# Kernel optimization log

Measured on AMD Instinct MI355X. Metric: run time of the kernel, lower is better.

The kernel has to match this reference:

```python
import jax, jax.numpy as jnp
import numpy as np

SEQ = 512; WIN = [4, 4, 4]; INNER = 5; DM = 256; H = 4; DK = 64; NEG = -1e9

def _all_sizes():
    s = [SEQ]
    for w in WIN:
        s.append(s[-1] // w)
    return s

def _build_mask():
    # Pyraformer get_mask: intra-scale band (inner_size) + inter-scale parent/child links.
    sizes = _all_sizes(); N = sum(sizes)
    starts = np.cumsum([0] + sizes)
    allow = np.zeros((N, N), bool)
    iw = INNER // 2
    for li, sz in enumerate(sizes):
        st = int(starts[li])
        for i in range(st, st + sz):
            allow[i, max(i - iw, st):min(i + iw + 1, st + sz)] = True
    for li in range(1, len(sizes)):
        st = int(starts[li])
        for i in range(st, st + sizes[li]):
            ls = int(starts[li - 1]) + (i - st) * WIN[li - 1]
            rs = st if i == st + sizes[li] - 1 else int(starts[li - 1]) + (i - st + 1) * WIN[li - 1]
            allow[i, ls:rs] = True
            allow[ls:rs, i] = True
    return jnp.asarray(~allow)  # True = blocked

def _build_indexes():
    # Pyraformer refer_points: for each base position, index of its node at every scale.
    sizes = _all_sizes(); starts = np.cumsum([0] + sizes)
    idx = np.zeros((SEQ, len(sizes)), np.int32)
    for i in range(SEQ):
        cur = i
        idx[i, 0] = cur
        for j in range(1, len(sizes)):
            inner = cur - int(starts[j - 1])
            cur = int(starts[j]) + min(inner // WIN[j - 1], sizes[j] - 1)
            idx[i, j] = cur
    return jnp.asarray(idx)

def _pos_enc(L, D):
    pos = np.arange(L)[:, None]
    div = np.exp(np.arange(0, D, 2) * (-np.log(10000.0) / D))
    pe = np.zeros((L, D), np.float32)
    pe[:, 0::2] = np.sin(pos * div)
    pe[:, 1::2] = np.cos(pos * div)
    return jnp.asarray(pe)

MASK = _build_mask()
INDEXES = _build_indexes()
PE = _pos_enc(SEQ, DM)
DN = ('NCH', 'OIH', 'NCH')

def _ln(x, g, b, eps=1e-5):
    m = x.mean(-1, keepdims=True)
    v = ((x - m) ** 2).mean(-1, keepdims=True)
    return (x - m) * jax.lax.rsqrt(v + eps) * g + b

def _forward(x_enc, x_mark, W_val, W_time, b_time, W_down, b_down, W_conv, b_conv, bn_g, bn_b, W_up, b_up, ln_c_g, ln_c_b, Wq, bq, Wk, bk, Wv, bv, Wo, bo, ln1_g, ln1_b, W1f, b1f, W2f, b2f, ln2_g, ln2_b, Wp, bp):
    B = x_enc.shape[0]
    # DataEmbedding: circular k=3 token conv + time-feature linear + fixed positional
    xt = jnp.pad(x_enc.transpose(0, 2, 1), ((0, 0), (0, 0), (1, 1)), mode='wrap')
    val = jax.lax.conv_general_dilated(xt, W_val, (1,), 'VALID', dimension_numbers=DN).transpose(0, 2, 1)
    emb = val + x_mark @ W_time + b_time + PE[None]  # [B, SEQ, DM]
    # CSCM Bottleneck_Construct: down-proj, strided conv pooling per scale, up-proj, concat, LN
    t = (emb @ W_down + b_down).transpose(0, 2, 1)  # [B, 64, SEQ]
    pooled = []
    for i in range(len(WIN)):
        t = jax.lax.conv_general_dilated(t, W_conv[i], (WIN[i],), 'VALID', dimension_numbers=DN) + b_conv[i][None, :, None]
        t = jax.nn.elu(t * bn_g[i][None, :, None] + bn_b[i][None, :, None])
        pooled.append(t)
    pooled = jnp.concatenate(pooled, axis=2).transpose(0, 2, 1) @ W_up + b_up  # [B, 168, DM]
    x = _ln(jnp.concatenate([emb, pooled], axis=1), ln_c_g, ln_c_b)  # [B, 680, DM]
    N = x.shape[1]
    scale = np.float32(1.0 / np.sqrt(DK))
    for l in range(Wq.shape[0]):
        q = (x @ Wq[l] + bq[l]).reshape(B, N, H, DK).transpose(0, 2, 1, 3)
        k = (x @ Wk[l] + bk[l]).reshape(B, N, H, DK).transpose(0, 2, 1, 3)
        v = (x @ Wv[l] + bv[l]).reshape(B, N, H, DK).transpose(0, 2, 1, 3)
        s = jnp.einsum('bhqd,bhkd->bhqk', q, k) * scale
        s = jnp.where(MASK[None, None], NEG, s)
        o = jnp.einsum('bhqk,bhkd->bhqd', jax.nn.softmax(s, axis=-1), v)
        o = o.transpose(0, 2, 1, 3).reshape(B, N, DM) @ Wo[l] + bo[l]
        x = _ln(x + o, ln1_g[l], ln1_b[l])  # post-norm (normalize_before=False)
        f = jax.nn.relu(x @ W1f[l] + b1f[l]) @ W2f[l] + b2f[l]
        x = _ln(x + f, ln2_g[l], ln2_b[l])
    # FC decoder path: gather each position's multi-scale nodes, concat features
    gathered = x[:, INDEXES.reshape(-1)].reshape(B, SEQ, -1)  # [B, SEQ, 4*DM]
    return gathered[:, -1] @ Wp + bp  # [B, 96]

def setup_inputs() -> dict:
    key = jax.random.key(0)
    ks = iter(jax.random.split(key, 64))
    def w(shape, s=0.05):
        return jax.random.normal(next(ks), shape, jnp.float32) * s
    d = {}
    d['x_enc'] = jax.random.normal(next(ks), (32, SEQ, 1), jnp.float32)
    d['x_mark'] = jax.random.normal(next(ks), (32, SEQ, 4), jnp.float32)
    d['W_val'] = w((DM, 1, 3))
    d['W_time'] = w((4, DM)); d['b_time'] = jnp.zeros((DM,), jnp.float32)
    d['W_down'] = w((DM, 64)); d['b_down'] = jnp.zeros((64,), jnp.float32)
    d['W_conv'] = w((3, 64, 64, 4)); d['b_conv'] = jnp.zeros((3, 64), jnp.float32)
    d['bn_g'] = jnp.ones((3, 64), jnp.float32); d['bn_b'] = jnp.zeros((3, 64), jnp.float32)
    d['W_up'] = w((64, DM)); d['b_up'] = jnp.zeros((DM,), jnp.float32)
    d['ln_c_g'] = jnp.ones((DM,), jnp.float32); d['ln_c_b'] = jnp.zeros((DM,), jnp.float32)
    d['Wq'] = w((2, DM, DM)); d['bq'] = jnp.zeros((2, DM), jnp.float32)
    d['Wk'] = w((2, DM, DM)); d['bk'] = jnp.zeros((2, DM), jnp.float32)
    d['Wv'] = w((2, DM, DM)); d['bv'] = jnp.zeros((2, DM), jnp.float32)
    d['Wo'] = w((2, DM, DM)); d['bo'] = jnp.zeros((2, DM), jnp.float32)
    d['ln1_g'] = jnp.ones((2, DM), jnp.float32); d['ln1_b'] = jnp.zeros((2, DM), jnp.float32)
    d['W1f'] = w((2, DM, 512)); d['b1f'] = jnp.zeros((2, 512), jnp.float32)
    d['W2f'] = w((2, 512, DM)); d['b2f'] = jnp.zeros((2, DM), jnp.float32)
    d['ln2_g'] = jnp.ones((2, DM), jnp.float32); d['ln2_b'] = jnp.zeros((2, DM), jnp.float32)
    d['Wp'] = w((4 * DM, 96)); d['bp'] = jnp.zeros((96,), jnp.float32)
    return d

def reference(x_enc, x_mark, W_val, W_time, b_time, W_down, b_down, W_conv, b_conv, bn_g, bn_b, W_up, b_up, ln_c_g, ln_c_b, Wq, bq, Wk, bk, Wv, bv, Wo, bo, ln1_g, ln1_b, W1f, b1f, W2f, b2f, ln2_g, ln2_b, Wp, bp):
    return _forward(x_enc, x_mark, W_val, W_time, b_time, W_down, b_down, W_conv, b_conv, bn_g, bn_b, W_up, b_up, ln_c_g, ln_c_b, Wq, bq, Wk, bk, Wv, bv, Wo, bo, ln1_g, ln1_b, W1f, b1f, W2f, b2f, ln2_g, ln2_b, Wp, bp)
```

## Files before the change

### kernel.cpp

```cpp
#include <hip/hip_runtime.h>
#include <hip/hip_bf16.h>
#include <math.h>

#define B 32
#define SEQ 512
#define NTOK 680
#define DM 256
#define FF 512
#define NROWS (B*NTOK)

using bf16x8 = __attribute__((ext_vector_type(8))) short;
using f32x4  = __attribute__((ext_vector_type(4))) float;
using u32x4  = __attribute__((ext_vector_type(4))) unsigned int;
typedef __hip_bfloat16 bf16;

__device__ __forceinline__ unsigned short f2bf(float f) {
    union { float f; unsigned u; } x; x.f = f;
    unsigned r = (x.u + 0x7fffu + ((x.u >> 16) & 1u)) >> 16;
    return (unsigned short)r;
}
__device__ __forceinline__ float bfu2f(unsigned short u) {
    union { unsigned u; float f; } x; x.u = ((unsigned)u) << 16;
    return x.f;
}
__device__ __forceinline__ void dotu(unsigned a, unsigned b, float& s) {
    union { unsigned u; float f; } al, ah, bl, bh;
    al.u = a << 16; ah.u = a & 0xffff0000u;
    bl.u = b << 16; bh.u = b & 0xffff0000u;
    s = fmaf(al.f, bl.f, s);
    s = fmaf(ah.f, bh.f, s);
}

__global__ __launch_bounds__(256) void emb_kernel(
    const float* __restrict__ x_enc, const float* __restrict__ x_mark,
    const float* __restrict__ W_val, const float* __restrict__ W_time,
    const float* __restrict__ b_time, float* __restrict__ X, bf16* __restrict__ Xe)
{
    int bs = blockIdx.x;
    int b = bs >> 9, s = bs & 511;
    int d = threadIdx.x;
    int sm1 = (s + 511) & 511, sp1 = (s + 1) & 511;
    float x0 = x_enc[b*512 + sm1];
    float x1 = x_enc[b*512 + s];
    float x2 = x_enc[b*512 + sp1];
    float val = x0 * W_val[d*3+0] + x1 * W_val[d*3+1] + x2 * W_val[d*3+2];
    const float* mk = &x_mark[(size_t)bs*4];
    float tm = mk[0]*W_time[d] + mk[1]*W_time[256+d] + mk[2]*W_time[512+d] + mk[3]*W_time[768+d];
    int i2 = d & ~1;
    float div = expf((float)i2 * (-9.210340371976184f / 256.0f));
    float ang = (float)s * div;
    float pe = (d & 1) ? cosf(ang) : sinf(ang);
    float out = val + tm + b_time[d] + pe;
    X[((size_t)(b*NTOK + s))*DM + d] = out;
    ((unsigned short*)Xe)[(size_t)bs*DM + d] = f2bf(out);
}

__global__ __launch_bounds__(64) void conv_kernel(
    const float* __restrict__ in, int inRPB, int inOff,
    float* __restrict__ Pool, int outOff, int Lout,
    const float* __restrict__ W_conv, const float* __restrict__ b_conv,
    const float* __restrict__ bn_g, const float* __restrict__ bn_b, int sc)
{
    __shared__ float lds[256];
    int blk = blockIdx.x;
    int b = blk / Lout, p = blk % Lout;
    int t = threadIdx.x;
    for (int u = t; u < 256; u += 64)
        lds[u] = in[((size_t)(b*inRPB + inOff + p*4 + (u >> 6)))*64 + (u & 63)];
    __syncthreads();
    float acc = b_conv[sc*64 + t];
    const float* w = &W_conv[(size_t)(sc*64 + t)*256];
    #pragma unroll 4
    for (int ci = 0; ci < 64; ++ci) {
        #pragma unroll
        for (int tap = 0; tap < 4; ++tap)
            acc = fmaf(lds[tap*64 + ci], w[ci*4 + tap], acc);
    }
    float v = acc * bn_g[sc*64 + t] + bn_b[sc*64 + t];
    v = v > 0.f ? v : expm1f(v);
    Pool[((size_t)(b*168 + outOff + p))*64 + t] = v;
}

__global__ __launch_bounds__(256) void up_kernel(
    const float* __restrict__ Pool, const float* __restrict__ W_up,
    const float* __restrict__ b_up, float* __restrict__ X)
{
    __shared__ float row[64];
    int blk = blockIdx.x;
    int b = blk / 168, p = blk % 168;
    int d = threadIdx.x;
    if (d < 64) row[d] = Pool[(size_t)blk*64 + d];
    __syncthreads();
    float acc = b_up[d];
    #pragma unroll 8
    for (int k = 0; k < 64; ++k) acc = fmaf(row[k], W_up[k*256 + d], acc);
    X[((size_t)(b*NTOK + 512 + p))*DM + d] = acc;
}

__global__ __launch_bounds__(256) void ln_kernel(
    const float* __restrict__ Xf, bf16* __restrict__ Xio,
    const float* __restrict__ g, const float* __restrict__ bta)
{
    int r = blockIdx.x*4 + (threadIdx.x >> 6);
    int lane = threadIdx.x & 63;
    float4 v = ((const float4*)(Xf + (size_t)r*DM))[lane];
    float s = v.x + v.y + v.z + v.w;
    #pragma unroll
    for (int o = 32; o; o >>= 1) s += __shfl_xor(s, o);
    float mean = s * (1.0f/256.0f);
    float dx = v.x-mean, dy = v.y-mean, dz = v.z-mean, dw = v.w-mean;
    float q = dx*dx + dy*dy + dz*dz + dw*dw;
    #pragma unroll
    for (int o = 32; o; o >>= 1) q += __shfl_xor(q, o);
    float inv = rsqrtf(q*(1.0f/256.0f) + 1e-5f);
    float4 gg = ((const float4*)g)[lane];
    float4 bb = ((const float4*)bta)[lane];
    float ox = dx*inv*gg.x + bb.x;
    float oy = dy*inv*gg.y + bb.y;
    float oz = dz*inv*gg.z + bb.z;
    float ow = dw*inv*gg.w + bb.w;
    unsigned u0 = (unsigned)f2bf(ox) | ((unsigned)f2bf(oy) << 16);
    unsigned u1 = (unsigned)f2bf(oz) | ((unsigned)f2bf(ow) << 16);
    ((uint2*)(Xio + (size_t)r*DM))[lane] = make_uint2(u0, u1);
}

__global__ void nbr_kernel(int* __restrict__ nbr, int* __restrict__ ncnt)
{
    int i = blockIdx.x * 64 + threadIdx.x;
    if (i >= NTOK) return;
    const int starts[5] = {0, 512, 640, 672, 680};
    int si = (i < 512) ? 0 : (i < 640) ? 1 : (i < 672) ? 2 : 3;
    int st = starts[si], en = starts[si+1];
    int idx = i - st;
    int cnt = 0;
    if (si >= 1) {
        int cs = starts[si-1] + idx*4;
        #pragma unroll
        for (int c = 0; c < 4; ++c) nbr[i*16 + cnt++] = cs + c;
    }
    int lo = (i-2 > st) ? i-2 : st;
    int hi = (i+2 < en-1) ? i+2 : en-1;
    for (int j = lo; j <= hi; ++j) nbr[i*16 + cnt++] = j;
    if (si <= 2) nbr[i*16 + cnt++] = starts[si+1] + (idx >> 2);
    ncnt[i] = cnt;
}

__global__ __launch_bounds__(256) void attn_kernel(
    const bf16* __restrict__ Q, const bf16* __restrict__ K,
    const bf16* __restrict__ V, bf16* __restrict__ O,
    const int* __restrict__ nbr, const int* __restrict__ ncnt)
{
    __shared__ float wsm[4][16];
    __shared__ int   jsm[4][16];
    int flat = blockIdx.x;
    int row = (flat & 7) * (NROWS/8) + (flat >> 3);
    int n = row % NTOK, b = row / NTOK;
    int h = threadIdx.x >> 6;
    int lane = threadIdx.x & 63;
    int j = lane >> 2, g = lane & 3;
    int cnt = ncnt[n];
    int nj = (j < cnt) ? nbr[n*16 + j] : n;
    int jr = b*NTOK + nj;

    const uint4* qp = (const uint4*)(Q + (size_t)row*DM + h*64 + g*16);
    const uint4* kp = (const uint4*)(K + (size_t)jr*DM + h*64 + g*16);
    uint4 qa = qp[0], qb = qp[1];
    uint4 ka = kp[0], kb = kp[1];
    float s = 0.f;
    dotu(qa.x, ka.x, s); dotu(qa.y, ka.y, s); dotu(qa.z, ka.z, s); dotu(qa.w, ka.w, s);
    dotu(qb.x, kb.x, s); dotu(qb.y, kb.y, s); dotu(qb.z, kb.z, s); dotu(qb.w, kb.w, s);
    s += __shfl_xor(s, 1);
    s += __shfl_xor(s, 2);
    s *= 0.125f;
    if (j >= cnt) s = -1e30f;
    float m = s;
    #pragma unroll
    for (int o = 4; o < 64; o <<= 1) m = fmaxf(m, __shfl_xor(m, o));
    float w = (j < cnt) ? expf(s - m) : 0.f;
    float den = w;
    #pragma unroll
    for (int o = 4; o < 64; o <<= 1) den += __shfl_xor(den, o);
    if (g == 0) { wsm[h][j] = w / den; jsm[h][j] = jr; }
    __syncthreads();

    float acc = 0.f;
    const unsigned short* Vu = (const unsigned short*)V;
    for (int jj = 0; jj < cnt; ++jj) {
        float wv = wsm[h][jj];
        int rr = jsm[h][jj];
        acc = fmaf(wv, bfu2f(Vu[(size_t)rr*DM + h*64 + lane]), acc);
    }
    ((unsigned short*)O)[(size_t)row*DM + h*64 + lane] = f2bf(acc);
}

struct WDesc { const float* src; bf16* dst; int K; int N; };
struct WTable { WDesc d[13]; };
__global__ __launch_bounds__(256) void wconv_kernel(WTable tbl)
{
    __shared__ float lds[32][33];
    WDesc ds = tbl.d[blockIdx.y];
    int ntn = ds.N >> 5;
    int ntiles = (ds.K >> 5) * ntn;
    int tile = blockIdx.x;
    if (tile >= ntiles) return;
    int k0 = (tile / ntn) * 32, n0 = (tile % ntn) * 32;
    int t = threadIdx.x;
    int r = t >> 3, c4 = (t & 7) * 4;
    float4 v = *(const float4*)(ds.src + (size_t)(k0 + r)*ds.N + n0 + c4);
    lds[r][c4+0] = v.x; lds[r][c4+1] = v.y; lds[r][c4+2] = v.z; lds[r][c4+3] = v.w;
    __syncthreads();
    unsigned u0 = (unsigned)f2bf(lds[c4+0][r]) | ((unsigned)f2bf(lds[c4+1][r]) << 16);
    unsigned u1 = (unsigned)f2bf(lds[c4+2][r]) | ((unsigned)f2bf(lds[c4+3][r]) << 16);
    *(uint2*)((unsigned short*)ds.dst + (size_t)(n0 + r)*ds.K + k0 + c4) = make_uint2(u0, u1);
}

__global__ __launch_bounds__(256) void wpt_kernel(
    const float* __restrict__ Wp, float* __restrict__ WpT)
{
    int e = blockIdx.x*256 + threadIdx.x;
    int o = e % 96, k = e / 96;
    WpT[(size_t)o*1024 + k] = Wp[(size_t)k*96 + o];
}

__global__ __launch_bounds__(512, 2) void qkv_kernel(
    const bf16* __restrict__ Xh,
    const bf16* __restrict__ WqT, const bf16* __restrict__ WkT, const bf16* __restrict__ WvT,
    const float* __restrict__ bq, const float* __restrict__ bk, const float* __restrict__ bv,
    bf16* __restrict__ Qh, bf16* __restrict__ Kh, bf16* __restrict__ Vh)
{
    __shared__ __align__(16) char smem[16384 + 16896];
    uint4* AsU = (uint4*)smem;
    const bf16x8* Asv = (const bf16x8*)smem;
    unsigned short* ctb = (unsigned short*)(smem + 16384);

    int t = threadIdx.x;
    int lane = t & 63, w = t >> 6;
    int nwg = gridDim.x;
    int wg = (blockIdx.x & 7) * (nwg >> 3) + (blockIdx.x >> 3);
    int row0 = wg * 32;
    const unsigned short* Xu = (const unsigned short*)Xh;

    #pragma unroll
    for (int i = 0; i < 2; ++i) {
        int gg = t + i*512, r = gg >> 5, c = gg & 31;
        AsU[r*32 + (c ^ (r & 7))] = *(const uint4*)(Xu + (size_t)(row0 + r)*DM + c*8);
    }
    __syncthreads();

    #pragma unroll
    for (int z = 0; z < 3; ++z) {
        const unsigned short* Wu = (const unsigned short*)((z == 0) ? WqT : (z == 1) ? WkT : WvT);
        const float* bias = (z == 0) ? bq : (z == 1) ? bk : bv;
        bf16* Op = (z == 0) ? Qh : (z == 1) ? Kh : Vh;

        f32x4 acc[2][2];
        #pragma unroll
        for (int m = 0; m < 2; ++m)
            #pragma unroll
            for (int nn = 0; nn < 2; ++nn)
                #pragma unroll
                for (int q = 0; q < 4; ++q) acc[m][nn][q] = 0.f;
        float bv_[2];
        #pragma unroll
        for (int nn = 0; nn < 2; ++nn) bv_[nn] = bias[w*32 + nn*16 + (lane & 15)];

        #pragma unroll
        for (int kh = 0; kh < 2; ++kh) {
            bf16x8 pw[8];
            #pragma unroll
            for (int i = 0; i < 8; ++i) {
                int kt = kh*128 + (i >> 1)*32, nn = i & 1;
                int nrow = w*32 + nn*16 + (lane & 15);
                pw[i] = *(const bf16x8*)(Wu + (size_t)nrow*256 + kt + (lane >> 4)*8);
            }
            #pragma unroll
            for (int ki = 0; ki < 4; ++ki) {
                int kt = kh*128 + ki*32;
                int cg = (kt >> 3) + (lane >> 4);
                bf16x8 af[2];
                #pragma unroll
                for (int m = 0; m < 2; ++m) {
                    int ar = m*16 + (lane & 15);
                    af[m] = Asv[ar*32 + (cg ^ (ar & 7))];
                }
                #pragma unroll
                for (int nn = 0; nn < 2; ++nn)
                    #pragma unroll
                    for (int m = 0; m < 2; ++m)
                        acc[m][nn] = __builtin_amdgcn_mfma_f32_16x16x32_bf16(af[m], pw[ki*2+nn], acc[m][nn], 0, 0, 0);
            }
        }

        __syncthreads();
        #pragma unroll
        for (int m = 0; m < 2; ++m)
            #pragma unroll
            for (int nn = 0; nn < 2; ++nn) {
                int col = w*32 + nn*16 + (lane & 15);
                #pragma unroll
                for (int q = 0; q < 4; ++q) {
                    int row = m*16 + (lane >> 4)*4 + q;
                    ctb[row*264 + col] = f2bf(acc[m][nn][q] + bv_[nn]);
                }
            }
        __syncthreads();
        #pragma unroll
        for (int i = 0; i < 2; ++i) {
            int idx = t + i*512;
            int row = idx >> 5, c16 = idx & 31;
            u32x4 uv = *(const u32x4*)(ctb + row*264 + c16*8);
            *(u32x4*)((unsigned short*)Op + (size_t)(row0 + row)*DM + c16*8) = uv;
        }
    }
}

#define CSTR 260
#define HSTR2 520
__global__ __launch_bounds__(512, 2) void layer2_kernel(
    const bf16* __restrict__ Ob, bf16* __restrict__ Xh,
    const bf16* __restrict__ WoT, const float* __restrict__ bo,
    const float* __restrict__ g1, const float* __restrict__ b1n,
    const bf16* __restrict__ W1t, const float* __restrict__ b1,
    const bf16* __restrict__ W2t, const float* __restrict__ b2,
    const float* __restrict__ g2, const float* __restrict__ b2n)
{
    __shared__ __align__(16) char smem[16384 + 33280];
    uint4* AsU = (uint4*)smem;
    const bf16x8* Asv = (const bf16x8*)smem;
    unsigned short* Asu16 = (unsigned short*)smem;
    float* ctile = (float*)(smem + 16384);
    unsigned short* hT = (unsigned short*)(smem + 16384);

    int t = threadIdx.x;
    int lane = t & 63, w = t >> 6;
    int nwg = gridDim.x;
    int wg = (blockIdx.x & 7) * (nwg >> 3) + (blockIdx.x >> 3);
    int row0 = wg * 32;
    const unsigned short* Obu = (const unsigned short*)Ob;
    const unsigned short* Xu  = (const unsigned short*)Xh;
    const unsigned short* WoU = (const unsigned short*)WoT;
    const unsigned short* W1u = (const unsigned short*)W1t;
    const unsigned short* W2u = (const unsigned short*)W2t;

    #pragma unroll
    for (int i = 0; i < 2; ++i) {
        int gg = t + i*512, r = gg >> 5, c = gg & 31;
        AsU[r*32 + (c ^ (r & 7))] = *(const uint4*)(Obu + (size_t)(row0 + r)*DM + c*8);
    }
    __syncthreads();

    {
        f32x4 acc[2][2];
        #pragma unroll
        for (int m = 0; m < 2; ++m)
            #pragma unroll
            for (int nn = 0; nn < 2; ++nn)
                #pragma unroll
                for (int q = 0; q < 4; ++q) acc[m][nn][q] = 0.f;
        float bvv[2];
        #pragma unroll
        for (int nn = 0; nn < 2; ++nn) bvv[nn] = bo[w*32 + nn*16 + (lane & 15)];

        #pragma unroll
        for (int kh = 0; kh < 2; ++kh) {
            bf16x8 pw[8];
            #pragma unroll
            for (int i = 0; i < 8; ++i) {
                int kt = kh*128 + (i >> 1)*32, nn = i & 1;
                int nrow = w*32 + nn*16 + (lane & 15);
                pw[i] = *(const bf16x8*)(WoU + (size_t)nrow*256 + kt + (lane >> 4)*8);
            }
            #pragma unroll
            for (int ki = 0; ki < 4; ++ki) {
                int kt = kh*128 + ki*32;
                int cg = (kt >> 3) + (lane >> 4);
                bf16x8 af[2];
                #pragma unroll
                for (int m = 0; m < 2; ++m) {
                    int ar = m*16 + (lane & 15);
                    af[m] = Asv[ar*32 + (cg ^ (ar & 7))];
                }
                #pragma unroll
                for (int nn = 0; nn < 2; ++nn)
                    #pragma unroll
                    for (int m = 0; m < 2; ++m)
                        acc[m][nn] = __builtin_amdgcn_mfma_f32_16x16x32_bf16(af[m], pw[ki*2+nn], acc[m][nn], 0, 0, 0);
            }
        }

        #pragma unroll
        for (int m = 0; m < 2; ++m)
            #pragma unroll
            for (int nn = 0; nn < 2; ++nn) {
                int col = w*32 + nn*16 + (lane & 15);
                #pragma unroll
                for (int q = 0; q < 4; ++q) {
                    int row = m*16 + (lane >> 4)*4 + q;
                    ctile[row*CSTR + col] = acc[m][nn][q] + bvv[nn];
                }
            }
    }
    __syncthreads();

    #pragma unroll
    for (int rr = 0; rr < 4; ++rr) {
        int row = w*4 + rr;
        float4 v = *(const float4*)(ctile + row*CSTR + lane*4);
        uint2 xu = *(const uint2*)(Xu + (size_t)(row0 + row)*DM + lane*4);
        v.x += bfu2f((unsigned short)(xu.x & 0xffffu));
        v.y += bfu2f((unsigned short)(xu.x >> 16));
        v.z += bfu2f((unsigned short)(xu.y & 0xffffu));
        v.w += bfu2f((unsigned short)(xu.y >> 16));
        float s = v.x + v.y + v.z + v.w;
        #pragma unroll
        for (int o = 32; o; o >>= 1) s += __shfl_xor(s, o);
        float mean = s * (1.0f/256.0f);
        float dx = v.x-mean, dy = v.y-mean, dz = v.z-mean, dw = v.w-mean;
        float q2 = dx*dx + dy*dy + dz*dz + dw*dw;
        #pragma unroll
        for (int o = 32; o; o >>= 1) q2 += __shfl_xor(q2, o);
        float inv = rsqrtf(q2*(1.0f/256.0f) + 1e-5f);
        float4 gg = ((const float4*)g1)[lane];
        float4 bb = ((const float4*)b1n)[lane];
        float ox = dx*inv*gg.x + bb.x;
        float oy = dy*inv*gg.y + bb.y;
        float oz = dz*inv*gg.z + bb.z;
        float ow = dw*inv*gg.w + bb.w;
        unsigned u0 = (unsigned)f2bf(ox) | ((unsigned)f2bf(oy) << 16);
        unsigned u1 = (unsigned)f2bf(oz) | ((unsigned)f2bf(ow) << 16);
        *(uint2*)(Asu16 + row*256 + (((lane>>1) ^ (row & 7))*8) + (lane & 1)*4) = make_uint2(u0, u1);
    }
    __syncthreads();

    f32x4 acc1[2][2][2];
    #pragma unroll
    for (int hf = 0; hf < 2; ++hf)
        #pragma unroll
        for (int m = 0; m < 2; ++m)
            #pragma unroll
            for (int nn = 0; nn < 2; ++nn)
                #pragma unroll
                for (int q = 0; q < 4; ++q) acc1[hf][m][nn][q] = 0.f;

    #pragma unroll
    for (int hf = 0; hf < 2; ++hf) {
        #pragma unroll
        for (int kh = 0; kh < 2; ++kh) {
            bf16x8 pw[8];
            #pragma unroll
            for (int i = 0; i < 8; ++i) {
                int kt = kh*128 + (i >> 1)*32, nn = i & 1;
                int nrow = hf*256 + w*32 + nn*16 + (lane & 15);
                pw[i] = *(const bf16x8*)(W1u + (size_t)nrow*256 + kt + (lane >> 4)*8);
            }
            #pragma unroll
            for (int ki = 0; ki < 4; ++ki) {
                int kt = kh*128 + ki*32;
                int cg = (kt >> 3) + (lane >> 4);
                bf16x8 af[2];
                #pragma unroll
                for (int m = 0; m < 2; ++m) {
                    int ar = m*16 + (lane & 15);
                    af[m] = Asv[ar*32 + (cg ^ (ar & 7))];
                }
                #pragma unroll
                for (int nn = 0; nn < 2; ++nn)
                    #pragma unroll
                    for (int m = 0; m < 2; ++m)
                        acc1[hf][m][nn] = __builtin_amdgcn_mfma_f32_16x16x32_bf16(af[m], pw[ki*2+nn], acc1[hf][m][nn], 0, 0, 0);
            }
        }
    }
    #pragma unroll
    for (int hf = 0; hf < 2; ++hf) {
        float b1v[2];
        #pragma unroll
        for (int nn = 0; nn < 2; ++nn) b1v[nn] = b1[hf*256 + w*32 + nn*16 + (lane & 15)];
        #pragma unroll
        for (int m = 0; m < 2; ++m)
            #pragma unroll
            for (int nn = 0; nn < 2; ++nn) {
                int col = hf*256 + w*32 + nn*16 + (lane & 15);
                #pragma unroll
                for (int q = 0; q < 4; ++q) {
                    int row = m*16 + (lane >> 4)*4 + q;
                    hT[row*HSTR2 + col] = f2bf(fmaxf(acc1[hf][m][nn][q] + b1v[nn], 0.f));
                }
            }
    }
    __syncthreads();

    f32x4 acc2[2][2];
    #pragma unroll
    for (int m = 0; m < 2; ++m)
        #pragma unroll
        for (int nn = 0; nn < 2; ++nn)
            #pragma unroll
            for (int q = 0; q < 4; ++q) acc2[m][nn][q] = 0.f;
    float b2v[2];
    #pragma unroll
    for (int nn = 0; nn < 2; ++nn) b2v[nn] = b2[w*32 + nn*16 + (lane & 15)];

    #pragma unroll
    for (int kh = 0; kh < 4; ++kh) {
        bf16x8 pw[8];
        #pragma unroll
        for (int i = 0; i < 8; ++i) {
            int kt = kh*128 + (i >> 1)*32, nn = i & 1;
            int nrow = w*32 + nn*16 + (lane & 15);
            pw[i] = *(const bf16x8*)(W2u + (size_t)nrow*512 + kt + (lane >> 4)*8);
        }
        #pragma unroll
        for (int ki = 0; ki < 4; ++ki) {
            int kt = kh*128 + ki*32;
            bf16x8 af[2];
            #pragma unroll
            for (int m = 0; m < 2; ++m) {
                int ar = m*16 + (lane & 15);
                af[m] = *(const bf16x8*)(hT + ar*HSTR2 + kt + (lane >> 4)*8);
            }
            #pragma unroll
            for (int nn = 0; nn < 2; ++nn)
                #pragma unroll
                for (int m = 0; m < 2; ++m)
                    acc2[m][nn] = __builtin_amdgcn_mfma_f32_16x16x32_bf16(af[m], pw[ki*2+nn], acc2[m][nn], 0, 0, 0);
        }
    }
    __syncthreads();

    #pragma unroll
    for (int m = 0; m < 2; ++m)
        #pragma unroll
        for (int nn = 0; nn < 2; ++nn) {
            int col = w*32 + nn*16 + (lane & 15);
            #pragma unroll
            for (int q = 0; q < 4; ++q) {
                int row = m*16 + (lane >> 4)*4 + q;
                ctile[row*CSTR + col] = acc2[m][nn][q] + b2v[nn];
            }
        }
    __syncthreads();
    #pragma unroll
    for (int rr = 0; rr < 4; ++rr) {
        int row = w*4 + rr;
        float4 v = *(const float4*)(ctile + row*CSTR + lane*4);
        uint2 xu = *(const uint2*)(Asu16 + row*256 + (((lane>>1) ^ (row & 7))*8) + (lane & 1)*4);
        v.x += bfu2f((unsigned short)(xu.x & 0xffffu));
        v.y += bfu2f((unsigned short)(xu.x >> 16));
        v.z += bfu2f((unsigned short)(xu.y & 0xffffu));
        v.w += bfu2f((unsigned short)(xu.y >> 16));
        float s = v.x + v.y + v.z + v.w;
        #pragma unroll
        for (int o = 32; o; o >>= 1) s += __shfl_xor(s, o);
        float mean = s * (1.0f/256.0f);
        float dx = v.x-mean, dy = v.y-mean, dz = v.z-mean, dw = v.w-mean;
        float q2 = dx*dx + dy*dy + dz*dz + dw*dw;
        #pragma unroll
        for (int o = 32; o; o >>= 1) q2 += __shfl_xor(q2, o);
        float inv = rsqrtf(q2*(1.0f/256.0f) + 1e-5f);
        float4 gg = ((const float4*)g2)[lane];
        float4 bb = ((const float4*)b2n)[lane];
        float ox = dx*inv*gg.x + bb.x;
        float oy = dy*inv*gg.y + bb.y;
        float oz = dz*inv*gg.z + bb.z;
        float ow = dw*inv*gg.w + bb.w;
        unsigned u0 = (unsigned)f2bf(ox) | ((unsigned)f2bf(oy) << 16);
        unsigned u1 = (unsigned)f2bf(oz) | ((unsigned)f2bf(ow) << 16);
        *(uint2*)((unsigned short*)Xh + (size_t)(row0 + row)*DM + lane*4) = make_uint2(u0, u1);
    }
}

__global__ __launch_bounds__(256) void mfma_gemm_dn(
    const bf16* __restrict__ A, const bf16* __restrict__ Wt,
    const float* __restrict__ bias, float* __restrict__ Op)
{
    __shared__ __align__(16) char smem[34816];
    uint4* AsU = (uint4*)smem;
    uint4* BsU = (uint4*)(smem + 16384);
    const bf16x8* Asv = (const bf16x8*)smem;
    const bf16x8* Bsv = (const bf16x8*)(smem + 16384);
    const int KD = 256, Nc = 64;

    int t = threadIdx.x;
    int lane = t & 63, wid = t >> 6;
    int wm = wid >> 1, wn = wid & 1;
    int nwg = gridDim.x;
    int wg = (blockIdx.x & 7) * (nwg >> 3) + (blockIdx.x >> 3);
    int row0 = wg * 128;
    int n0 = 0;

    f32x4 acc[4][2];
    #pragma unroll
    for (int i = 0; i < 4; ++i)
        #pragma unroll
        for (int jn = 0; jn < 2; ++jn)
            #pragma unroll
            for (int r = 0; r < 4; ++r) acc[i][jn][r] = 0.f;

    uint4 pa[4], pb[2];
    #pragma unroll
    for (int i = 0; i < 4; ++i) {
        int gg = t + i*256, r = gg >> 3, c = gg & 7;
        pa[i] = *reinterpret_cast<const uint4*>(A + (size_t)(row0 + r)*KD + c*8);
    }
    #pragma unroll
    for (int i = 0; i < 2; ++i) {
        int gg = t + i*256, r = gg >> 3, c = gg & 7;
        pb[i] = *reinterpret_cast<const uint4*>(Wt + (size_t)(n0 + r)*KD + c*8);
    }

    #pragma unroll
    for (int kt = 0; kt < KD; kt += 64) {
        __syncthreads();
        #pragma unroll
        for (int i = 0; i < 4; ++i) {
            int gg = t + i*256, r = gg >> 3, c = gg & 7;
            AsU[r*8 + (c ^ (r & 7))] = pa[i];
        }
        #pragma unroll
        for (int i = 0; i < 2; ++i) {
            int gg = t + i*256, r = gg >> 3, c = gg & 7;
            BsU[r*8 + (c ^ (r & 7))] = pb[i];
        }
        __syncthreads();
        if (kt + 64 < KD) {
            #pragma unroll
            for (int i = 0; i < 4; ++i) {
                int gg = t + i*256, r = gg >> 3, c = gg & 7;
                pa[i] = *reinterpret_cast<const uint4*>(A + (size_t)(row0 + r)*KD + (kt + 64) + c*8);
            }
            #pragma unroll
            for (int i = 0; i < 2; ++i) {
                int gg = t + i*256, r = gg >> 3, c = gg & 7;
                pb[i] = *reinterpret_cast<const uint4*>(Wt + (size_t)(n0 + r)*KD + (kt + 64) + c*8);
            }
        }
        #pragma unroll
        for (int ks = 0; ks < 2; ++ks) {
            int cg = ks*4 + (lane >> 4);
            bf16x8 af[4], bfr[2];
            #pragma unroll
            for (int m = 0; m < 4; ++m) {
                int ar = wm*64 + m*16 + (lane & 15);
                af[m] = Asv[ar*8 + (cg ^ (ar & 7))];
            }
            #pragma unroll
            for (int nn = 0; nn < 2; ++nn) {
                int br = wn*32 + nn*16 + (lane & 15);
                bfr[nn] = Bsv[br*8 + (cg ^ (br & 7))];
            }
            #pragma unroll
            for (int m = 0; m < 4; ++m)
                #pragma unroll
                for (int nn = 0; nn < 2; ++nn)
                    acc[m][nn] = __builtin_amdgcn_mfma_f32_16x16x32_bf16(af[m], bfr[nn], acc[m][nn], 0, 0, 0);
        }
    }

    __syncthreads();
    float* ctile = (float*)smem;
    #pragma unroll
    for (int m = 0; m < 4; ++m) {
        #pragma unroll
        for (int nn = 0; nn < 2; ++nn) {
            int cc = wn*32 + nn*16 + (lane & 15);
            float bcol = bias[n0 + cc];
            #pragma unroll
            for (int r = 0; r < 4; ++r) {
                int rr = wm*64 + m*16 + (lane >> 4)*4 + r;
                ctile[rr*68 + cc] = acc[m][nn][r] + bcol;
            }
        }
    }
    __syncthreads();
    int c4 = (t & 15) * 4;
    #pragma unroll
    for (int rr = t >> 4; rr < 128; rr += 16) {
        float4 v = *reinterpret_cast<const float4*>(ctile + rr*68 + c4);
        *reinterpret_cast<float4*>(Op + (size_t)(row0 + rr)*Nc + n0 + c4) = v;
    }
}

__global__ __launch_bounds__(512) void final_kernel(
    const bf16* __restrict__ Xh, const float* __restrict__ WpT,
    const float* __restrict__ bp, float* __restrict__ out)
{
    __shared__ float rows[1024];
    int b = blockIdx.x, t = threadIdx.x;
    int lane = t & 63, w = t >> 6;
    const unsigned short* Xu = (const unsigned short*)Xh;
    for (int u = t; u < 1024; u += 512) {
        int g = u >> 8;
        int id = (g == 0) ? 511 : (g == 1) ? 639 : (g == 2) ? 671 : 679;
        rows[u] = bfu2f(Xu[((size_t)(b*NTOK + id))*DM + (u & 255)]);
    }
    __syncthreads();
    #pragma unroll
    for (int oi = 0; oi < 12; ++oi) {
        int o = w*12 + oi;
        float acc = 0.f;
        #pragma unroll
        for (int i = 0; i < 16; ++i) {
            int k = i*64 + lane;
            acc = fmaf(rows[k], WpT[(size_t)o*1024 + k], acc);
        }
        #pragma unroll
        for (int off = 32; off; off >>= 1) acc += __shfl_xor(acc, off);
        if (lane == 0) out[b*96 + o] = acc + bp[o];
    }
}

extern "C" void kernel_launch(void* const* d_in, const int* in_sizes, int n_in,
                              void* d_out, int out_size, void* d_ws, size_t ws_size,
                              hipStream_t stream)
{
    const float* x_enc  = (const float*)d_in[0];
    const float* x_mark = (const float*)d_in[1];
    const float* W_val  = (const float*)d_in[2];
    const float* W_time = (const float*)d_in[3];
    const float* b_time = (const float*)d_in[4];
    const float* W_down = (const float*)d_in[5];
    const float* b_down = (const float*)d_in[6];
    const float* W_conv = (const float*)d_in[7];
    const float* b_conv = (const float*)d_in[8];
    const float* bn_g   = (const float*)d_in[9];
    const float* bn_b   = (const float*)d_in[10];
    const float* W_up   = (const float*)d_in[11];
    const float* b_up   = (const float*)d_in[12];
    const float* ln_c_g = (const float*)d_in[13];
    const float* ln_c_b = (const float*)d_in[14];
    const float* Wq     = (const float*)d_in[15];
    const float* bq     = (const float*)d_in[16];
    const float* Wk     = (const float*)d_in[17];
    const float* bk     = (const float*)d_in[18];
    const float* Wv     = (const float*)d_in[19];
    const float* bv     = (const float*)d_in[20];
    const float* Wo     = (const float*)d_in[21];
    const float* bo     = (const float*)d_in[22];
    const float* ln1_g  = (const float*)d_in[23];
    const float* ln1_b  = (const float*)d_in[24];
    const float* W1f    = (const float*)d_in[25];
    const float* b1f    = (const float*)d_in[26];
    const float* W2f    = (const float*)d_in[27];
    const float* b2f    = (const float*)d_in[28];
    const float* ln2_g  = (const float*)d_in[29];
    const float* ln2_b  = (const float*)d_in[30];
    const float* Wp     = (const float*)d_in[31];
    const float* bp     = (const float*)d_in[32];

    const size_t RB = (size_t)NROWS * DM;
    float* ws = (float*)d_ws;
    float* X    = ws;
    float* Td   = X + RB;
    float* Pool = Td + (size_t)B*SEQ*64;
    float* WpT  = Pool + (size_t)B*168*64;
    bf16* bws   = (bf16*)(WpT + 96*1024);
    bf16* Xh   = bws;
    bf16* Qh   = Xh  + RB;
    bf16* Kh   = Qh  + RB;
    bf16* Vh   = Kh  + RB;
    bf16* Obh  = Vh  + RB;
    bf16* Xe   = Obh + RB;
    bf16* WqT  = Xe  + (size_t)B*SEQ*DM;
    bf16* WkT  = WqT + 2*65536;
    bf16* WvT  = WkT + 2*65536;
    bf16* WoT  = WvT + 2*65536;
    bf16* W1T  = WoT + 2*65536;
    bf16* W2T  = W1T + 2*131072;
    bf16* WdT  = W2T + 2*131072;
    int*  nbr  = (int*)(WdT + 64*256);
    int*  ncnt = nbr + NTOK*16;

    WTable tbl;
    for (int l = 0; l < 2; ++l) {
        tbl.d[l*6+0] = { Wq  + (size_t)l*65536,  WqT + (size_t)l*65536,  256, 256 };
        tbl.d[l*6+1] = { Wk  + (size_t)l*65536,  WkT + (size_t)l*65536,  256, 256 };
        tbl.d[l*6+2] = { Wv  + (size_t)l*65536,  WvT + (size_t)l*65536,  256, 256 };
        tbl.d[l*6+3] = { Wo  + (size_t)l*65536,  WoT + (size_t)l*65536,  256, 256 };
        tbl.d[l*6+4] = { W1f + (size_t)l*131072, W1T + (size_t)l*131072, 256, 512 };
        tbl.d[l*6+5] = { W2f + (size_t)l*131072, W2T + (size_t)l*131072, 512, 256 };
    }
    tbl.d[12] = { W_down, WdT, 256, 64 };
    wconv_kernel<<<dim3(128, 13), 256, 0, stream>>>(tbl);
    wpt_kernel<<<384, 256, 0, stream>>>(Wp, WpT);

    emb_kernel<<<B*SEQ, 256, 0, stream>>>(x_enc, x_mark, W_val, W_time, b_time, X, Xe);
    mfma_gemm_dn<<<128, 256, 0, stream>>>(Xe, WdT, b_down, Td);
    conv_kernel<<<B*128, 64, 0, stream>>>(Td, 512, 0,   Pool, 0,   128, W_conv, b_conv, bn_g, bn_b, 0);
    conv_kernel<<<B*32,  64, 0, stream>>>(Pool, 168, 0,  Pool, 128, 32,  W_conv, b_conv, bn_g, bn_b, 1);
    conv_kernel<<<B*8,   64, 0, stream>>>(Pool, 168, 128,Pool, 160, 8,   W_conv, b_conv, bn_g, bn_b, 2);
    up_kernel<<<B*168, 256, 0, stream>>>(Pool, W_up, b_up, X);
    ln_kernel<<<NROWS/4, 256, 0, stream>>>(X, Xh, ln_c_g, ln_c_b);
    nbr_kernel<<<11, 64, 0, stream>>>(nbr, ncnt);

    for (int l = 0; l < 2; ++l) {
        const bf16* wqt = WqT + (size_t)l*65536;
        const bf16* wkt = WkT + (size_t)l*65536;
        const bf16* wvt = WvT + (size_t)l*65536;
        const bf16* wot = WoT + (size_t)l*65536;
        const bf16* w1t = W1T + (size_t)l*131072;
        const bf16* w2t = W2T + (size_t)l*131072;
        const float* bq_ = bq + l*DM; const float* bk_ = bk + l*DM;
        const float* bv_ = bv + l*DM; const float* bo_ = bo + l*DM;
        const float* b1_ = b1f + l*FF; const float* b2_ = b2f + l*DM;

        qkv_kernel<<<680, 512, 0, stream>>>(Xh, wqt, wkt, wvt, bq_, bk_, bv_, Qh, Kh, Vh);
        attn_kernel<<<NROWS, 256, 0, stream>>>(Qh, Kh, Vh, Obh, nbr, ncnt);
        layer2_kernel<<<680, 512, 0, stream>>>(Obh, Xh, wot, bo_,
            ln1_g + l*DM, ln1_b + l*DM, w1t, b1_, w2t, b2_, ln2_g + l*DM, ln2_b + l*DM);
    }

    final_kernel<<<B, 512, 0, stream>>>(Xh, WpT, bp, (float*)d_out);
}
```

Measured before the change: 389.1 us.

## Fuse sparse neighbor attention into the output-projection/FFN layer kernel

Removes the standalone attention kernel and computes the masked neighbor attention for each 32-row tile directly inside the layer kernel, writing the results straight into the swizzled LDS A-tile. Each wave handles four rows across all heads, passing weights and neighbor indices with lane shuffles instead of shared memory. This drops a kernel launch and the global write and read of the attention output buffer. The cost is a serial attention phase at the start of the GEMM kernel, with only 680 workgroups, which may hurt latency hiding compared with the row-per-block attention launch.

```diff
diff --git a/kernel.cpp b/kernel.cpp
--- a/kernel.cpp
+++ b/kernel.cpp
@@ -145,54 +145,6 @@
     ncnt[i] = cnt;
 }
 
-__global__ __launch_bounds__(256) void attn_kernel(
-    const bf16* __restrict__ Q, const bf16* __restrict__ K,
-    const bf16* __restrict__ V, bf16* __restrict__ O,
-    const int* __restrict__ nbr, const int* __restrict__ ncnt)
-{
-    __shared__ float wsm[4][16];
-    __shared__ int   jsm[4][16];
-    int flat = blockIdx.x;
-    int row = (flat & 7) * (NROWS/8) + (flat >> 3);
-    int n = row % NTOK, b = row / NTOK;
-    int h = threadIdx.x >> 6;
-    int lane = threadIdx.x & 63;
-    int j = lane >> 2, g = lane & 3;
-    int cnt = ncnt[n];
-    int nj = (j < cnt) ? nbr[n*16 + j] : n;
-    int jr = b*NTOK + nj;
-
-    const uint4* qp = (const uint4*)(Q + (size_t)row*DM + h*64 + g*16);
-    const uint4* kp = (const uint4*)(K + (size_t)jr*DM + h*64 + g*16);
-    uint4 qa = qp[0], qb = qp[1];
-    uint4 ka = kp[0], kb = kp[1];
-    float s = 0.f;
-    dotu(qa.x, ka.x, s); dotu(qa.y, ka.y, s); dotu(qa.z, ka.z, s); dotu(qa.w, ka.w, s);
-    dotu(qb.x, kb.x, s); dotu(qb.y, kb.y, s); dotu(qb.z, kb.z, s); dotu(qb.w, kb.w, s);
-    s += __shfl_xor(s, 1);
-    s += __shfl_xor(s, 2);
-    s *= 0.125f;
-    if (j >= cnt) s = -1e30f;
-    float m = s;
-    #pragma unroll
-    for (int o = 4; o < 64; o <<= 1) m = fmaxf(m, __shfl_xor(m, o));
-    float w = (j < cnt) ? expf(s - m) : 0.f;
-    float den = w;
-    #pragma unroll
-    for (int o = 4; o < 64; o <<= 1) den += __shfl_xor(den, o);
-    if (g == 0) { wsm[h][j] = w / den; jsm[h][j] = jr; }
-    __syncthreads();
-
-    float acc = 0.f;
-    const unsigned short* Vu = (const unsigned short*)V;
-    for (int jj = 0; jj < cnt; ++jj) {
-        float wv = wsm[h][jj];
-        int rr = jsm[h][jj];
-        acc = fmaf(wv, bfu2f(Vu[(size_t)rr*DM + h*64 + lane]), acc);
-    }
-    ((unsigned short*)O)[(size_t)row*DM + h*64 + lane] = f2bf(acc);
-}
-
 struct WDesc { const float* src; bf16* dst; int K; int N; };
 struct WTable { WDesc d[13]; };
 __global__ __launch_bounds__(256) void wconv_kernel(WTable tbl)
@@ -316,13 +268,15 @@
 
 #define CSTR 260
 #define HSTR2 520
-__global__ __launch_bounds__(512, 2) void layer2_kernel(
-    const bf16* __restrict__ Ob, bf16* __restrict__ Xh,
+__global__ __launch_bounds__(512, 2) void layerfull_kernel(
+    const bf16* __restrict__ Qh, const bf16* __restrict__ Kh, const bf16* __restrict__ Vh,
+    bf16* __restrict__ Xh,
     const bf16* __restrict__ WoT, const float* __restrict__ bo,
     const float* __restrict__ g1, const float* __restrict__ b1n,
     const bf16* __restrict__ W1t, const float* __restrict__ b1,
     const bf16* __restrict__ W2t, const float* __restrict__ b2,
-    const float* __restrict__ g2, const float* __restrict__ b2n)
+    const float* __restrict__ g2, const float* __restrict__ b2n,
+    const int* __restrict__ nbr, const int* __restrict__ ncnt)
 {
     __shared__ __align__(16) char smem[16384 + 33280];
     uint4* AsU = (uint4*)smem;
@@ -336,16 +290,59 @@
     int nwg = gridDim.x;
     int wg = (blockIdx.x & 7) * (nwg >> 3) + (blockIdx.x >> 3);
     int row0 = wg * 32;
-    const unsigned short* Obu = (const unsigned short*)Ob;
+    const unsigned short* Qu = (const unsigned short*)Qh;
+    const unsigned short* Ku = (const unsigned short*)Kh;
+    const unsigned short* Vu = (const unsigned short*)Vh;
     const unsigned short* Xu  = (const unsigned short*)Xh;
     const unsigned short* WoU = (const unsigned short*)WoT;
     const unsigned short* W1u = (const unsigned short*)W1t;
     const unsigned short* W2u = (const unsigned short*)W2t;
 
-    #pragma unroll
-    for (int i = 0; i < 2; ++i) {
-        int gg = t + i*512, r = gg >> 5, c = gg & 31;
-        AsU[r*32 + (c ^ (r & 7))] = *(const uint4*)(Obu + (size_t)(row0 + r)*DM + c*8);
+    {
+        int j = lane >> 2, g = lane & 3;
+        #pragma unroll
+        for (int rr = 0; rr < 4; ++rr) {
+            int row = w*4 + rr;
+            int grow = row0 + row;
+            int n = grow % NTOK, b = grow / NTOK;
+            int cnt = ncnt[n];
+            int nj = (j < cnt) ? nbr[n*16 + j] : n;
+            int jr = b*NTOK + nj;
+            float p[4];
+            #pragma unroll
+            for (int h = 0; h < 4; ++h) {
+                const uint4* qp = (const uint4*)(Qu + (size_t)grow*DM + h*64 + g*16);
+                const uint4* kp = (const uint4*)(Ku + (size_t)jr*DM + h*64 + g*16);
+                uint4 qa = qp[0], qb = qp[1];
+                uint4 ka = kp[0], kb = kp[1];
+                float s = 0.f;
+                dotu(qa.x, ka.x, s); dotu(qa.y, ka.y, s); dotu(qa.z, ka.z, s); dotu(qa.w, ka.w, s);
+                dotu(qb.x, kb.x, s); dotu(qb.y, kb.y, s); dotu(qb.z, kb.z, s); dotu(qb.w, kb.w, s);
+                s += __shfl_xor(s, 1);
+                s += __shfl_xor(s, 2);
+                s *= 0.125f;
+                if (j >= cnt) s = -1e30f;
+                float m = s;
+                #pragma unroll
+                for (int o = 4; o < 64; o <<= 1) m = fmaxf(m, __shfl_xor(m, o));
+                float wgt = (j < cnt) ? expf(s - m) : 0.f;
+                float den = wgt;
+                #pragma unroll
+                for (int o = 4; o < 64; o <<= 1) den += __shfl_xor(den, o);
+                p[h] = wgt / den;
+            }
+            #pragma unroll
+            for (int h = 0; h < 4; ++h) {
+                float acc = 0.f;
+                for (int jj = 0; jj < cnt; ++jj) {
+                    float wv = __shfl(p[h], jj*4);
+                    int rr2 = __shfl(jr, jj*4);
+                    acc = fmaf(wv, bfu2f(Vu[(size_t)rr2*DM + h*64 + lane]), acc);
+                }
+                int col = h*64 + lane;
+                Asu16[row*256 + (((col >> 3) ^ (row & 7))*8) + (col & 7)] = f2bf(acc);
+            }
+        }
     }
     __syncthreads();
 
@@ -759,8 +756,7 @@
     bf16* Qh   = Xh  + RB;
     bf16* Kh   = Qh  + RB;
     bf16* Vh   = Kh  + RB;
-    bf16* Obh  = Vh  + RB;
-    bf16* Xe   = Obh + RB;
+    bf16* Xe   = Vh  + RB;
     bf16* WqT  = Xe  + (size_t)B*SEQ*DM;
     bf16* WkT  = WqT + 2*65536;
     bf16* WvT  = WkT + 2*65536;
@@ -805,9 +801,9 @@
         const float* b1_ = b1f + l*FF; const float* b2_ = b2f + l*DM;
 
         qkv_kernel<<<680, 512, 0, stream>>>(Xh, wqt, wkt, wvt, bq_, bk_, bv_, Qh, Kh, Vh);
-        attn_kernel<<<NROWS, 256, 0, stream>>>(Qh, Kh, Vh, Obh, nbr, ncnt);
-        layer2_kernel<<<680, 512, 0, stream>>>(Obh, Xh, wot, bo_,
-            ln1_g + l*DM, ln1_b + l*DM, w1t, b1_, w2t, b2_, ln2_g + l*DM, ln2_b + l*DM);
+        layerfull_kernel<<<680, 512, 0, stream>>>(Qh, Kh, Vh, Xh, wot, bo_,
+            ln1_g + l*DM, ln1_b + l*DM, w1t, b1_, w2t, b2_, ln2_g + l*DM, ln2_b + l*DM,
+            nbr, ncnt);
     }
 
     final_kernel<<<B, 512, 0, stream>>>(Xh, WpT, bp, (float*)d_out);
```

After: 534.0 us. 1.37x slower.
